# Kernel tuning notes

Measured on AMD Instinct MI355X. Metric: run time of the kernel, lower is better.

Reference implementation:

```python
import jax, jax.numpy as jnp
import numpy as np

B, T, D, E, L, MAXP, PRED, TOPK = 128, 2048, 256, 32, 8, 168, 168, 2
INIT_STD = 0.02


def setup_inputs() -> dict:
    key = jax.random.key(0)
    ks = jax.random.split(key, 18)
    n = jax.random.normal
    s = INIT_STD
    inp = {
        "ctx_embed": n(ks[0], (B, T, D), jnp.float32),
        "query_experts": n(ks[1], (E, MAXP, D), jnp.float32) * s,
        "query_pos": n(ks[2], (MAXP, D), jnp.float32) * s,
        "len_emb": n(ks[3], (MAXP + 1, D), jnp.float32),  # nn.Embedding table
        "latents": n(ks[4], (L, D), jnp.float32) * s,
        "w_lat_q": n(ks[5], (D, D), jnp.float32) / np.sqrt(D),
        "w_ctx_k": n(ks[6], (D, D), jnp.float32) / np.sqrt(D),
        "w_ctx_v": n(ks[7], (D, D), jnp.float32) / np.sqrt(D),
        "w_lat_out": n(ks[8], (D, D), jnp.float32) / np.sqrt(D),
        "w_step_q": n(ks[9], (D, D), jnp.float32) / np.sqrt(D),
        "w_lat_k": n(ks[10], (D, D), jnp.float32) / np.sqrt(D),
        "w_lat_v": n(ks[11], (D, D), jnp.float32) / np.sqrt(D),
        "w_step_out": n(ks[12], (D, D), jnp.float32) / np.sqrt(D),
        "gate_w1": n(ks[13], (2 * D, D), jnp.float32) / np.sqrt(2 * D),
        "gate_b1": jnp.zeros((D,), jnp.float32),
        "gate_w2": n(ks[14], (D, E), jnp.float32) / np.sqrt(D),
        "gate_b2": jnp.zeros((E,), jnp.float32),
        "pred_len": PRED,
    }
    return inp


def _sdpa_1head(q, k, v):
    # q: [B,Q,D], k/v: [B,K,D]; single-head scaled dot-product attention
    scale = jnp.asarray(q.shape[-1], q.dtype) ** -0.5
    attn = jax.nn.softmax(jnp.einsum('bqd,bkd->bqk', q, k) * scale, axis=-1)
    return jnp.einsum('bqk,bkd->bqd', attn, v)


def reference(ctx_embed, query_experts, query_pos, len_emb, latents,
              w_lat_q, w_ctx_k, w_ctx_v, w_lat_out,
              w_step_q, w_lat_k, w_lat_v, w_step_out,
              gate_w1, gate_b1, gate_w2, gate_b2, pred_len):
    Bb, Tt, Dd = ctx_embed.shape
    P = pred_len

    # step base: positional queries + pred-length embedding
    pos = query_pos[:P][None]                      # [1,P,D]
    len_vec = len_emb[P][None, None]               # [1,1,D]
    step_base = jnp.broadcast_to(pos + len_vec, (Bb, P, Dd))

    # latent <- context cross-attention
    lat = jnp.broadcast_to(latents[None], (Bb, latents.shape[0], Dd))
    q1 = lat @ w_lat_q
    k1 = ctx_embed @ w_ctx_k
    v1 = ctx_embed @ w_ctx_v
    lat_ctx = _sdpa_1head(q1, k1, v1) @ w_lat_out  # [B,L,D]

    # step <- latent cross-attention
    q2 = step_base @ w_step_q
    k2 = lat_ctx @ w_lat_k
    v2 = lat_ctx @ w_lat_v
    step_ctx = _sdpa_1head(q2, k2, v2) @ w_step_out  # [B,P,D]

    # gating MLP over [step_base, step_ctx]
    gate_inp = jnp.concatenate([step_base, step_ctx], axis=-1)  # [B,P,2D]
    h = jax.nn.gelu(gate_inp @ gate_w1 + gate_b1, approximate=False)
    logits = h @ gate_w2 + gate_b2                               # [B,P,E]

    # top-k masking + softmax (keep top-k logits, others -> -inf)
    topv = jax.lax.top_k(logits, TOPK)[0]
    kth = topv[..., -1:]
    masked = jnp.where(logits >= kth, logits, -jnp.inf)
    weights = jax.nn.softmax(masked, axis=-1)                    # [B,P,E]

    # mixture of expert queries (einsum avoids [B,P,E,D] intermediate)
    queries = jnp.einsum('bpe,epd->bpd', weights, query_experts[:, :P, :])
    return queries
```

## Files before the change

### kernel.cpp

```cpp
#include <hip/hip_runtime.h>
#include <math.h>

#define NB 128
#define NT 2048
#define ND 256
#define NE 32
#define NL 8
#define NP 168
#define SCL 0.0625f

#define OFF_QK   0
#define OFF_LATQ 2048
#define OFF_WVO  4096
#define OFF_WSO1 69632
#define OFF_WVW  135168
#define OFF_G0   200704
#define OFF_Q2S  243712
#define OFF_AV   286720
#define OFF_DEN  4481024
#define OFF_K2   4497408
#define OFF_VW   4759552

typedef __attribute__((ext_vector_type(8))) short short8b;
typedef __attribute__((ext_vector_type(4))) float f32x4;

static __device__ __forceinline__ unsigned short f2bf(float f){
  unsigned u = __float_as_uint(f);
  u += 0x7fffu + ((u >> 16) & 1u);
  return (unsigned short)(u >> 16);
}

static __device__ __forceinline__ short8b pack8(float4 lo, float4 hi){
  short8b r;
  r[0]=(short)f2bf(lo.x); r[1]=(short)f2bf(lo.y); r[2]=(short)f2bf(lo.z); r[3]=(short)f2bf(lo.w);
  r[4]=(short)f2bf(hi.x); r[5]=(short)f2bf(hi.y); r[6]=(short)f2bf(hi.z); r[7]=(short)f2bf(hi.w);
  return r;
}

__global__ __launch_bounds__(256) void pre1(const float* __restrict__ latents,
    const float* __restrict__ wlq, const float* __restrict__ wcv,
    const float* __restrict__ wlo, const float* __restrict__ wso,
    const float* __restrict__ gw1, const float* __restrict__ gb1,
    const float* __restrict__ qpos, const float* __restrict__ lemb,
    const float* __restrict__ wsq, float* __restrict__ ws)
{
  int bid = blockIdx.x, tid = threadIdx.x;
  if (bid < 256){
    const float* a = wcv + bid*ND;
    float acc = 0.f;
    #pragma unroll 8
    for (int k=0;k<ND;k++) acc += a[k]*wlo[k*ND+tid];
    ws[OFF_WVO + bid*ND + tid] = acc;
  } else if (bid < 512){
    int i = bid-256;
    const float* a = wso + i*ND;
    float acc = 0.f;
    #pragma unroll 8
    for (int k=0;k<ND;k++) acc += a[k]*gw1[(ND+k)*ND+tid];
    ws[OFF_WSO1 + i*ND + tid] = acc;
  } else if (bid < 512+NP){
    int p = bid-512;
    float ag = gb1[tid], aq = 0.f;
    #pragma unroll 4
    for (int j=0;j<ND;j++){
      float sb = qpos[p*ND+j] + lemb[NP*ND+j];
      ag += sb*gw1[j*ND+tid];
      aq += sb*wsq[j*ND+tid];
    }
    ws[OFF_G0  + p*ND + tid] = ag;
    ws[OFF_Q2S + p*ND + tid] = aq*SCL;
  } else {
    int l = bid-(512+NP);
    float acc = 0.f;
    #pragma unroll 8
    for (int m=0;m<ND;m++) acc += latents[l*ND+m]*wlq[m*ND+tid];
    ws[OFF_LATQ + l*ND + tid] = acc;
  }
}

__global__ __launch_bounds__(256) void pre2(const float* __restrict__ wck,
                                            const float* __restrict__ wlv,
                                            float* __restrict__ ws)
{
  int bid = blockIdx.x, tid = threadIdx.x;
  if (bid < 256){
    int d = bid;
    float wk = wck[d*ND + tid];
    float part[NL];
    #pragma unroll
    for (int l=0;l<NL;l++) part[l] = ws[OFF_LATQ + l*ND + tid]*wk;
    #pragma unroll
    for (int m=1;m<64;m<<=1){
      #pragma unroll
      for (int l=0;l<NL;l++) part[l] += __shfl_xor(part[l], m);
    }
    __shared__ float red[4][NL];
    if ((tid&63)==0){
      #pragma unroll
      for (int l=0;l<NL;l++) red[tid>>6][l] = part[l];
    }
    __syncthreads();
    if (tid < NL){
      float s = red[0][tid]+red[1][tid]+red[2][tid]+red[3][tid];
      ws[OFF_QK + tid*ND + d] = s*SCL;
    }
  } else {
    int dd = bid - 256;
    const float* a = wlv + dd*ND;
    float acc = 0.f;
    #pragma unroll 8
    for (int k=0;k<ND;k++) acc += a[k]*ws[OFF_WSO1 + k*ND + tid];
    ws[OFF_WVW + dd*ND + tid] = acc;
  }
}

__global__ __launch_bounds__(256) void kA(const float* __restrict__ ctx, float* __restrict__ ws)
{
  __shared__ float ctile[32*256];
  __shared__ float efull[128*8];

  int bid = blockIdx.x;
  int b = bid >> 4, sp = bid & 15;
  int tid = threadIdx.x;
  int wv = tid >> 6, lane = tid & 63;
  int c = lane & 15, g = lane >> 4;
  int dq = lane;
  int c7 = c & 7;

  short8b afrag[8];
  if (c < NL){
    const float* qk = ws + OFF_QK + c*ND + g*8;
    #pragma unroll
    for (int kk=0;kk<8;kk++){
      float4 lo = *(const float4*)(qk + kk*32);
      float4 hi = *(const float4*)(qk + kk*32 + 4);
      afrag[kk] = pack8(lo, hi);
    }
  } else {
    short8b z;
    #pragma unroll
    for (int j=0;j<8;j++) z[j] = 0;
    #pragma unroll
    for (int kk=0;kk<8;kk++) afrag[kk] = z;
  }

  float av[8][4];
  #pragma unroll
  for (int l=0;l<8;l++){
    #pragma unroll
    for (int j=0;j<4;j++) av[l][j] = 0.f;
  }

  const float* rbase = ctx + ((size_t)(b*NT + sp*128 + wv*8))*ND;
  float* myrows = ctile + wv*8*256;

  #pragma unroll 2
  for (int sub=0; sub<4; ++sub){
    const float* rs = rbase + (size_t)sub*32*ND;
    float4 st[8];
    #pragma unroll
    for (int i=0;i<8;i++)
      st[i] = *(const float4*)(rs + (size_t)i*ND + lane*4);
    #pragma unroll
    for (int i=0;i<8;i++)
      *(float4*)(myrows + i*256 + ((lane ^ i)<<2)) = st[i];

    f32x4 acc = {0.f,0.f,0.f,0.f};
    const float* brow = myrows + c7*256;
    #pragma unroll
    for (int kk=0;kk<8;kk++){
      int sA = 2*g + 8*kk;
      float4 lo = *(const float4*)(brow + (((sA  ) ^ c7)<<2));
      float4 hi = *(const float4*)(brow + (((sA+1) ^ c7)<<2));
      acc = __builtin_amdgcn_mfma_f32_16x16x32_bf16(afrag[kk], pack8(lo,hi), acc, 0, 0, 0);
    }
    if (g < 2 && c < 8){
      float4 ev = make_float4(__expf(acc[0]),__expf(acc[1]),__expf(acc[2]),__expf(acc[3]));
      *(float4*)&efull[(sub*32 + wv*8 + c)*8 + g*4] = ev;
    }

    #pragma unroll
    for (int i=0;i<8;i++){
      float4 c4 = *(const float4*)(myrows + i*256 + ((dq ^ i)<<2));
      const float* ep = efull + (sub*32 + wv*8 + i)*8;
      float4 e0 = *(const float4*)ep;
      float4 e1 = *(const float4*)(ep+4);
      av[0][0]+=e0.x*c4.x; av[0][1]+=e0.x*c4.y; av[0][2]+=e0.x*c4.z; av[0][3]+=e0.x*c4.w;
      av[1][0]+=e0.y*c4.x; av[1][1]+=e0.y*c4.y; av[1][2]+=e0.y*c4.z; av[1][3]+=e0.y*c4.w;
      av[2][0]+=e0.z*c4.x; av[2][1]+=e0.z*c4.y; av[2][2]+=e0.z*c4.z; av[2][3]+=e0.z*c4.w;
      av[3][0]+=e0.w*c4.x; av[3][1]+=e0.w*c4.y; av[3][2]+=e0.w*c4.z; av[3][3]+=e0.w*c4.w;
      av[4][0]+=e1.x*c4.x; av[4][1]+=e1.x*c4.y; av[4][2]+=e1.x*c4.z; av[4][3]+=e1.x*c4.w;
      av[5][0]+=e1.y*c4.x; av[5][1]+=e1.y*c4.y; av[5][2]+=e1.y*c4.z; av[5][3]+=e1.y*c4.w;
      av[6][0]+=e1.z*c4.x; av[6][1]+=e1.z*c4.y; av[6][2]+=e1.z*c4.z; av[6][3]+=e1.z*c4.w;
      av[7][0]+=e1.w*c4.x; av[7][1]+=e1.w*c4.y; av[7][2]+=e1.w*c4.z; av[7][3]+=e1.w*c4.w;
    }
  }

  __syncthreads();

  float* red = ctile;
  #pragma unroll
  for (int l=0;l<8;l++)
    *(float4*)(red + (((l*4 + wv)*64 + dq)<<2)) = make_float4(av[l][0],av[l][1],av[l][2],av[l][3]);

  if (wv == 0){
    float dpart[8];
    #pragma unroll
    for (int l=0;l<8;l++) dpart[l] = 0.f;
    #pragma unroll
    for (int q=0;q<2;q++){
      const float* ep = efull + (q*64 + lane)*8;
      float4 e0 = *(const float4*)ep;
      float4 e1 = *(const float4*)(ep+4);
      dpart[0]+=e0.x; dpart[1]+=e0.y; dpart[2]+=e0.z; dpart[3]+=e0.w;
      dpart[4]+=e1.x; dpart[5]+=e1.y; dpart[6]+=e1.z; dpart[7]+=e1.w;
    }
    #pragma unroll
    for (int m=1;m<64;m<<=1){
      #pragma unroll
      for (int l=0;l<8;l++) dpart[l] += __shfl_xor(dpart[l], m);
    }
    if (lane == 0){
      #pragma unroll
      for (int l=0;l<8;l++) ws[OFF_DEN + bid*8 + l] = dpart[l];
    }
  }
  __syncthreads();

  #pragma unroll
  for (int rep=0; rep<2; ++rep){
    int lidx = tid + rep*256;
    int l = lidx >> 6, d2 = lidx & 63;
    float4 s0 = *(const float4*)(red + (((l*4 + 0)*64 + d2)<<2));
    float4 s1 = *(const float4*)(red + (((l*4 + 1)*64 + d2)<<2));
    float4 s2 = *(const float4*)(red + (((l*4 + 2)*64 + d2)<<2));
    float4 s3 = *(const float4*)(red + (((l*4 + 3)*64 + d2)<<2));
    float4 o;
    o.x = s0.x+s1.x+s2.x+s3.x;
    o.y = s0.y+s1.y+s2.y+s3.y;
    o.z = s0.z+s1.z+s2.z+s3.z;
    o.w = s0.w+s1.w+s2.w+s3.w;
    *(float4*)&ws[OFF_AV + ((size_t)(bid*8 + l))*ND + d2*4] = o;
  }
}

__global__ __launch_bounds__(256) void kB1(const float* __restrict__ wlk,
                                           float* __restrict__ ws)
{
  int bid = blockIdx.x;
  int b = bid >> 1, half = bid & 1;
  int d = threadIdx.x;
  __shared__ float avnT[256][8];
  __shared__ float latT[256][8];

  float dent[8];
  #pragma unroll
  for (int l=0;l<8;l++) dent[l] = 0.f;
  #pragma unroll 4
  for (int sp=0;sp<16;sp++){
    const float* dp = ws + OFF_DEN + (size_t)(b*16+sp)*8;
    float4 d0 = *(const float4*)dp;
    float4 d1 = *(const float4*)(dp+4);
    dent[0]+=d0.x; dent[1]+=d0.y; dent[2]+=d0.z; dent[3]+=d0.w;
    dent[4]+=d1.x; dent[5]+=d1.y; dent[6]+=d1.z; dent[7]+=d1.w;
  }
  float av8[8];
  #pragma unroll
  for (int l=0;l<8;l++) av8[l] = 0.f;
  #pragma unroll 2
  for (int sp=0;sp<16;sp++){
    size_t base = OFF_AV + ((size_t)(b*16+sp))*8*ND + d;
    #pragma unroll
    for (int l=0;l<8;l++) av8[l] += ws[base + (size_t)l*ND];
  }
  #pragma unroll
  for (int l=0;l<8;l++) av8[l] /= dent[l];
  *(float4*)&avnT[d][0] = make_float4(av8[0],av8[1],av8[2],av8[3]);
  *(float4*)&avnT[d][4] = make_float4(av8[4],av8[5],av8[6],av8[7]);
  __syncthreads();

  float lc[8];
  #pragma unroll
  for (int l=0;l<8;l++) lc[l] = 0.f;
  #pragma unroll 8
  for (int dd=0;dd<ND;dd++){
    float w = ws[OFF_WVO + dd*ND + d];
    float4 a0 = *(const float4*)&avnT[dd][0];
    float4 a1 = *(const float4*)&avnT[dd][4];
    lc[0]+=a0.x*w; lc[1]+=a0.y*w; lc[2]+=a0.z*w; lc[3]+=a0.w*w;
    lc[4]+=a1.x*w; lc[5]+=a1.y*w; lc[6]+=a1.z*w; lc[7]+=a1.w*w;
  }
  *(float4*)&latT[d][0] = make_float4(lc[0],lc[1],lc[2],lc[3]);
  *(float4*)&latT[d][4] = make_float4(lc[4],lc[5],lc[6],lc[7]);
  __syncthreads();

  const float* w3 = half ? (ws + OFF_WVW) : wlk;
  float o8[8];
  #pragma unroll
  for (int l=0;l<8;l++) o8[l] = 0.f;
  #pragma unroll 8
  for (int dd=0;dd<ND;dd++){
    float w = w3[dd*ND + d];
    float4 a0 = *(const float4*)&latT[dd][0];
    float4 a1 = *(const float4*)&latT[dd][4];
    o8[0]+=a0.x*w; o8[1]+=a0.y*w; o8[2]+=a0.z*w; o8[3]+=a0.w*w;
    o8[4]+=a1.x*w; o8[5]+=a1.y*w; o8[6]+=a1.z*w; o8[7]+=a1.w*w;
  }
  size_t obase = (half ? OFF_VW : OFF_K2) + (size_t)b*8*ND + d;
  #pragma unroll
  for (int l=0;l<8;l++) ws[obase + l*ND] = o8[l];
}

__global__ __launch_bounds__(256) void kB2(const float* __restrict__ ws,
    const float* __restrict__ gw2, const float* __restrict__ gb2,
    const float* __restrict__ qe, float* __restrict__ out)
{
  int bid = blockIdx.x;
  int b = bid / 6, p0 = (bid % 6)*28;
  int tid = threadIdx.x;

  __shared__ float q2h[28][260];
  __shared__ float k2s[8][260];
  __shared__ float vws[8][260];
  __shared__ float wexp[28][8];
  __shared__ float lg[28][33];
  __shared__ float4 sel[28];

  #pragma unroll
  for (int i=0;i<7;i++){
    int idx = tid + i*256;
    int r = idx >> 6, c4 = idx & 63;
    *(float4*)&q2h[r][c4*4] = *(const float4*)&ws[OFF_Q2S + (p0+r)*ND + c4*4];
  }
  #pragma unroll
  for (int i=0;i<2;i++){
    int idx = tid + i*256;
    int l = idx >> 6, c4 = idx & 63;
    *(float4*)&k2s[l][c4*4] = *(const float4*)&ws[OFF_K2 + (size_t)(b*8+l)*ND + c4*4];
    *(float4*)&vws[l][c4*4] = *(const float4*)&ws[OFF_VW + (size_t)(b*8+l)*ND + c4*4];
  }
  __syncthreads();

  {
    int pp = tid >> 3, l1 = tid & 7;
    if (pp < 28){
      float s2 = 0.f;
      #pragma unroll 8
      for (int i=0;i<64;i++){
        float4 qa = *(const float4*)&q2h[pp][4*i];
        float4 kb = *(const float4*)&k2s[l1][4*i];
        s2 += qa.x*kb.x + qa.y*kb.y + qa.z*kb.z + qa.w*kb.w;
      }
      float e2 = __expf(s2);
      float den = e2;
      den += __shfl_xor(den,1); den += __shfl_xor(den,2); den += __shfl_xor(den,4);
      wexp[pp][l1] = e2/den;
    }
  }
  __syncthreads();

  {
    float vcol[8];
    #pragma unroll
    for (int l=0;l<8;l++) vcol[l] = vws[l][tid];
    #pragma unroll 4
    for (int p=0;p<28;p++){
      float4 w0 = *(const float4*)&wexp[p][0];
      float4 w1v = *(const float4*)&wexp[p][4];
      float x = ws[OFF_G0 + (p0+p)*ND + tid]
              + w0.x*vcol[0]+w0.y*vcol[1]+w0.z*vcol[2]+w0.w*vcol[3]
              + w1v.x*vcol[4]+w1v.y*vcol[5]+w1v.z*vcol[6]+w1v.w*vcol[7];
      q2h[p][tid] = 0.5f*x*(1.f+erff(x*0.70710678118654752f));
    }
  }
  __syncthreads();

  {
    int e = tid & 31, pq = tid >> 5;
    if (pq < 7){
      float b2v = gb2[e];
      float a0=b2v, a1=b2v, a2=b2v, a3=b2v;
      for (int cc=0;cc<ND;cc+=4){
        float w20 = gw2[(cc+0)*NE + e];
        float w21 = gw2[(cc+1)*NE + e];
        float w22 = gw2[(cc+2)*NE + e];
        float w23 = gw2[(cc+3)*NE + e];
        float4 h0 = *(const float4*)&q2h[pq*4+0][cc];
        float4 h1 = *(const float4*)&q2h[pq*4+1][cc];
        float4 h2 = *(const float4*)&q2h[pq*4+2][cc];
        float4 h3 = *(const float4*)&q2h[pq*4+3][cc];
        a0 += h0.x*w20 + h0.y*w21 + h0.z*w22 + h0.w*w23;
        a1 += h1.x*w20 + h1.y*w21 + h1.z*w22 + h1.w*w23;
        a2 += h2.x*w20 + h2.y*w21 + h2.z*w22 + h2.w*w23;
        a3 += h3.x*w20 + h3.y*w21 + h3.z*w22 + h3.w*w23;
      }
      lg[pq*4+0][e] = a0;
      lg[pq*4+1][e] = a1;
      lg[pq*4+2][e] = a2;
      lg[pq*4+3][e] = a3;
    }
  }
  __syncthreads();

  if (tid < 28){
    float m1 = -1e30f, m2 = -1e30f;
    int e1 = 0, ee2 = 0;
    for (int e3=0;e3<NE;e3++){
      float v = lg[tid][e3];
      if (v > m1){ m2 = m1; ee2 = e1; m1 = v; e1 = e3; }
      else if (v > m2){ m2 = v; ee2 = e3; }
    }
    float z = __expf(m2 - m1);
    float inv = 1.f/(1.f+z);
    sel[tid] = make_float4(__int_as_float(e1), __int_as_float(ee2), inv, z*inv);
  }
  __syncthreads();

  for (int p=0;p<28;p++){
    float4 s = sel[p];
    int e1 = __float_as_int(s.x), ee2 = __float_as_int(s.y);
    float q1v = qe[((size_t)e1*NP + (p0+p))*ND + tid];
    float q2v = qe[((size_t)ee2*NP + (p0+p))*ND + tid];
    out[((size_t)b*NP + (p0+p))*ND + tid] = s.z*q1v + s.w*q2v;
  }
}

extern "C" void kernel_launch(void* const* d_in, const int* in_sizes, int n_in,
                              void* d_out, int out_size, void* d_ws, size_t ws_size,
                              hipStream_t stream)
{
  const float* ctx  = (const float*)d_in[0];
  const float* qe   = (const float*)d_in[1];
  const float* qpos = (const float*)d_in[2];
  const float* lemb = (const float*)d_in[3];
  const float* lat  = (const float*)d_in[4];
  const float* wlq  = (const float*)d_in[5];
  const float* wck  = (const float*)d_in[6];
  const float* wcv  = (const float*)d_in[7];
  const float* wlo  = (const float*)d_in[8];
  const float* wsq  = (const float*)d_in[9];
  const float* wlk  = (const float*)d_in[10];
  const float* wlv  = (const float*)d_in[11];
  const float* wso  = (const float*)d_in[12];
  const float* gw1  = (const float*)d_in[13];
  const float* gb1  = (const float*)d_in[14];
  const float* gw2  = (const float*)d_in[15];
  const float* gb2  = (const float*)d_in[16];
  float* out = (float*)d_out;
  float* ws  = (float*)d_ws;

  pre1<<<512+NP+NL, 256, 0, stream>>>(lat, wlq, wcv, wlo, wso, gw1, gb1, qpos, lemb, wsq, ws);
  pre2<<<512, 256, 0, stream>>>(wck, wlv, ws);
  kA  <<<2048, 256, 0, stream>>>(ctx, ws);
  kB1 <<<NB*2, 256, 0, stream>>>(wlk, ws);
  kB2 <<<NB*6, 256, 0, stream>>>(ws, gw2, gb2, qe, out);
}
```

Before: 165.6 us.

## Use 512-thread kA blocks with register prefetch and in-register denominators

The context-attention kernel kA now runs 1024 blocks of 512 threads, each covering 256 context rows, instead of 2048 blocks of 256 threads. The next 8-row global tile is prefetched into registers while the current tile's MFMA and weighted-sum work proceeds. Softmax denominators are accumulated in registers per wave and reduced through a small shared array, replacing the separate shuffle reduction. The partial-result buffers halve, so kB1 sums 8 splits instead of 16 and the workspace offsets shrink. The cost is higher shared-memory and register use per block, which may lower occupancy.

After: 332.6 us. 101% more time.

```diff
diff --git a/kernel.cpp b/kernel.cpp
--- a/kernel.cpp
+++ b/kernel.cpp
@@ -17,9 +17,9 @@
 #define OFF_G0   200704
 #define OFF_Q2S  243712
 #define OFF_AV   286720
-#define OFF_DEN  4481024
-#define OFF_K2   4497408
-#define OFF_VW   4759552
+#define OFF_DEN  2383872
+#define OFF_K2   2392064
+#define OFF_VW   2654208
 
 typedef __attribute__((ext_vector_type(8))) short short8b;
 typedef __attribute__((ext_vector_type(4))) float f32x4;
@@ -114,18 +114,19 @@
   }
 }
 
-__global__ __launch_bounds__(256) void kA(const float* __restrict__ ctx, float* __restrict__ ws)
-{
-  __shared__ float ctile[32*256];
-  __shared__ float efull[128*8];
+__global__ __launch_bounds__(512,4) void kA(const float* __restrict__ ctx, float* __restrict__ ws)
+{
+  __shared__ float ctile[64*256];
+  __shared__ float ebuf[8][8][8];
+  __shared__ float denred[8][8];
 
   int bid = blockIdx.x;
-  int b = bid >> 4, sp = bid & 15;
+  int b = bid >> 3, sp = bid & 7;
   int tid = threadIdx.x;
   int wv = tid >> 6, lane = tid & 63;
   int c = lane & 15, g = lane >> 4;
+  int c7 = c & 7;
   int dq = lane;
-  int c7 = c & 7;
 
   short8b afrag[8];
   if (c < NL){
@@ -145,26 +146,31 @@
   }
 
   float av[8][4];
+  float den8[8];
   #pragma unroll
   for (int l=0;l<8;l++){
+    den8[l] = 0.f;
     #pragma unroll
     for (int j=0;j<4;j++) av[l][j] = 0.f;
   }
 
-  const float* rbase = ctx + ((size_t)(b*NT + sp*128 + wv*8))*ND;
+  const float* gw = ctx + ((size_t)(b*NT + sp*256 + wv*8))*ND + lane*4;
   float* myrows = ctile + wv*8*256;
 
-  #pragma unroll 2
+  float4 pf[8];
+  #pragma unroll
+  for (int i=0;i<8;i++) pf[i] = *(const float4*)(gw + (size_t)i*ND);
+
+  #pragma unroll 1
   for (int sub=0; sub<4; ++sub){
-    const float* rs = rbase + (size_t)sub*32*ND;
-    float4 st[8];
     #pragma unroll
     for (int i=0;i<8;i++)
-      st[i] = *(const float4*)(rs + (size_t)i*ND + lane*4);
-    #pragma unroll
-    for (int i=0;i<8;i++)
-      *(float4*)(myrows + i*256 + ((lane ^ i)<<2)) = st[i];
-
+      *(float4*)(myrows + i*256 + ((lane ^ i)<<2)) = pf[i];
+    if (sub < 3){
+      const float* gn = gw + (size_t)(sub+1)*64*ND;
+      #pragma unroll
+      for (int i=0;i<8;i++) pf[i] = *(const float4*)(gn + (size_t)i*ND);
+    }
     f32x4 acc = {0.f,0.f,0.f,0.f};
     const float* brow = myrows + c7*256;
     #pragma unroll
@@ -176,13 +182,12 @@
     }
     if (g < 2 && c < 8){
       float4 ev = make_float4(__expf(acc[0]),__expf(acc[1]),__expf(acc[2]),__expf(acc[3]));
-      *(float4*)&efull[(sub*32 + wv*8 + c)*8 + g*4] = ev;
-    }
-
+      *(float4*)&ebuf[wv][c][g*4] = ev;
+    }
     #pragma unroll
     for (int i=0;i<8;i++){
       float4 c4 = *(const float4*)(myrows + i*256 + ((dq ^ i)<<2));
-      const float* ep = efull + (sub*32 + wv*8 + i)*8;
+      const float* ep = &ebuf[wv][i][0];
       float4 e0 = *(const float4*)ep;
       float4 e1 = *(const float4*)(ep+4);
       av[0][0]+=e0.x*c4.x; av[0][1]+=e0.x*c4.y; av[0][2]+=e0.x*c4.z; av[0][3]+=e0.x*c4.w;
@@ -193,54 +198,38 @@
       av[5][0]+=e1.y*c4.x; av[5][1]+=e1.y*c4.y; av[5][2]+=e1.y*c4.z; av[5][3]+=e1.y*c4.w;
       av[6][0]+=e1.z*c4.x; av[6][1]+=e1.z*c4.y; av[6][2]+=e1.z*c4.z; av[6][3]+=e1.z*c4.w;
       av[7][0]+=e1.w*c4.x; av[7][1]+=e1.w*c4.y; av[7][2]+=e1.w*c4.z; av[7][3]+=e1.w*c4.w;
-    }
-  }
-
-  __syncthreads();
-
+      den8[0]+=e0.x; den8[1]+=e0.y; den8[2]+=e0.z; den8[3]+=e0.w;
+      den8[4]+=e1.x; den8[5]+=e1.y; den8[6]+=e1.z; den8[7]+=e1.w;
+    }
+  }
+
+  __syncthreads();
+
+  if (lane == 0){
+    #pragma unroll
+    for (int l=0;l<8;l++) denred[wv][l] = den8[l];
+  }
   float* red = ctile;
   #pragma unroll
   for (int l=0;l<8;l++)
-    *(float4*)(red + (((l*4 + wv)*64 + dq)<<2)) = make_float4(av[l][0],av[l][1],av[l][2],av[l][3]);
-
-  if (wv == 0){
-    float dpart[8];
-    #pragma unroll
-    for (int l=0;l<8;l++) dpart[l] = 0.f;
-    #pragma unroll
-    for (int q=0;q<2;q++){
-      const float* ep = efull + (q*64 + lane)*8;
-      float4 e0 = *(const float4*)ep;
-      float4 e1 = *(const float4*)(ep+4);
-      dpart[0]+=e0.x; dpart[1]+=e0.y; dpart[2]+=e0.z; dpart[3]+=e0.w;
-      dpart[4]+=e1.x; dpart[5]+=e1.y; dpart[6]+=e1.z; dpart[7]+=e1.w;
-    }
-    #pragma unroll
-    for (int m=1;m<64;m<<=1){
-      #pragma unroll
-      for (int l=0;l<8;l++) dpart[l] += __shfl_xor(dpart[l], m);
-    }
-    if (lane == 0){
-      #pragma unroll
-      for (int l=0;l<8;l++) ws[OFF_DEN + bid*8 + l] = dpart[l];
-    }
-  }
-  __syncthreads();
-
-  #pragma unroll
-  for (int rep=0; rep<2; ++rep){
-    int lidx = tid + rep*256;
-    int l = lidx >> 6, d2 = lidx & 63;
-    float4 s0 = *(const float4*)(red + (((l*4 + 0)*64 + d2)<<2));
-    float4 s1 = *(const float4*)(red + (((l*4 + 1)*64 + d2)<<2));
-    float4 s2 = *(const float4*)(red + (((l*4 + 2)*64 + d2)<<2));
-    float4 s3 = *(const float4*)(red + (((l*4 + 3)*64 + d2)<<2));
-    float4 o;
-    o.x = s0.x+s1.x+s2.x+s3.x;
-    o.y = s0.y+s1.y+s2.y+s3.y;
-    o.z = s0.z+s1.z+s2.z+s3.z;
-    o.w = s0.w+s1.w+s2.w+s3.w;
+    *(float4*)(red + (((l*8 + wv)*64 + dq)<<2)) = make_float4(av[l][0],av[l][1],av[l][2],av[l][3]);
+  __syncthreads();
+
+  {
+    int l = tid >> 6, d2 = tid & 63;
+    float4 o = make_float4(0.f,0.f,0.f,0.f);
+    #pragma unroll
+    for (int w=0; w<8; ++w){
+      float4 s = *(const float4*)(red + (((l*8 + w)*64 + d2)<<2));
+      o.x += s.x; o.y += s.y; o.z += s.z; o.w += s.w;
+    }
     *(float4*)&ws[OFF_AV + ((size_t)(bid*8 + l))*ND + d2*4] = o;
+  }
+  if (tid < NL){
+    float s = 0.f;
+    #pragma unroll
+    for (int w=0; w<8; ++w) s += denred[w][tid];
+    ws[OFF_DEN + bid*8 + tid] = s;
   }
 }
 
@@ -255,26 +244,20 @@
 
   float dent[8];
   #pragma unroll
-  for (int l=0;l<8;l++) dent[l] = 0.f;
-  #pragma unroll 4
-  for (int sp=0;sp<16;sp++){
-    const float* dp = ws + OFF_DEN + (size_t)(b*16+sp)*8;
-    float4 d0 = *(const float4*)dp;
-    float4 d1 = *(const float4*)(dp+4);
-    dent[0]+=d0.x; dent[1]+=d0.y; dent[2]+=d0.z; dent[3]+=d0.w;
-    dent[4]+=d1.x; dent[5]+=d1.y; dent[6]+=d1.z; dent[7]+=d1.w;
+  for (int l=0;l<8;l++){
+    float s = 0.f;
+    #pragma unroll
+    for (int sp=0;sp<8;sp++) s += ws[OFF_DEN + (b*8+sp)*8 + l];
+    dent[l] = s;
   }
   float av8[8];
   #pragma unroll
-  for (int l=0;l<8;l++) av8[l] = 0.f;
-  #pragma unroll 2
-  for (int sp=0;sp<16;sp++){
-    size_t base = OFF_AV + ((size_t)(b*16+sp))*8*ND + d;
-    #pragma unroll
-    for (int l=0;l<8;l++) av8[l] += ws[base + (size_t)l*ND];
-  }
-  #pragma unroll
-  for (int l=0;l<8;l++) av8[l] /= dent[l];
+  for (int l=0;l<8;l++){
+    float s = 0.f;
+    #pragma unroll
+    for (int sp=0;sp<8;sp++) s += ws[OFF_AV + ((size_t)((b*8+sp)*8 + l))*ND + d];
+    av8[l] = s / dent[l];
+  }
   *(float4*)&avnT[d][0] = make_float4(av8[0],av8[1],av8[2],av8[3]);
   *(float4*)&avnT[d][4] = make_float4(av8[4],av8[5],av8[6],av8[7]);
   __syncthreads();
@@ -451,7 +434,7 @@
 
   pre1<<<512+NP+NL, 256, 0, stream>>>(lat, wlq, wcv, wlo, wso, gw1, gb1, qpos, lemb, wsq, ws);
   pre2<<<512, 256, 0, stream>>>(wck, wlv, ws);
-  kA  <<<2048, 256, 0, stream>>>(ctx, ws);
+  kA  <<<NB*8, 512, 0, stream>>>(ctx, ws);
   kB1 <<<NB*2, 256, 0, stream>>>(wlk, ws);
   kB2 <<<NB*6, 256, 0, stream>>>(ws, gw2, gb2, qe, out);
 }
```
